# Kernel tuning notes

Measured on AMD Instinct MI355X. Metric: run time of the kernel, lower is better.

The kernel has to match this reference:

```python
import jax, jax.numpy as jnp
import numpy as np
from jax import lax

B, N, S, D1, D2 = 16, 4096, 1024, 128, 256
C_IN, C_MID, C_OUT = D1 + D2, 256, 128
BN_EPS = 1e-5


def setup_inputs() -> dict:
    key = jax.random.key(0)
    ks = jax.random.split(key, 12)
    return {
        "xyz1": jax.random.normal(ks[0], (B, N, 3), jnp.float32),
        "xyz2": jax.random.normal(ks[1], (B, S, 3), jnp.float32),
        "points1": jax.random.normal(ks[2], (B, N, D1), jnp.float32),
        "points2": jax.random.normal(ks[3], (B, S, D2), jnp.float32),
        # 1x1 Conv1d weights (kernel size 1 -> plain channel matmul)
        "W1": jax.random.normal(ks[4], (C_MID, C_IN), jnp.float32) * (1.0 / np.sqrt(C_IN)),
        "b1": jax.random.normal(ks[5], (C_MID,), jnp.float32) * 0.01,
        "g1": jnp.ones((C_MID,), jnp.float32),
        "be1": jnp.zeros((C_MID,), jnp.float32),
        "W2": jax.random.normal(ks[6], (C_OUT, C_MID), jnp.float32) * (1.0 / np.sqrt(C_MID)),
        "b2": jax.random.normal(ks[7], (C_OUT,), jnp.float32) * 0.01,
        "g2": jnp.ones((C_OUT,), jnp.float32),
        "be2": jnp.zeros((C_OUT,), jnp.float32),
    }


def _bn_relu(x, g, be):
    # BatchNorm1d in training mode: batch stats over (B, L) per channel, biased var
    mean = jnp.mean(x, axis=(0, 2), keepdims=True)
    var = jnp.var(x, axis=(0, 2), keepdims=True)
    y = (x - mean) * lax.rsqrt(var + BN_EPS)
    return jax.nn.relu(y * g[None, :, None] + be[None, :, None])


def reference(xyz1, xyz2, points1, points2, W1, b1, g1, be1, W2, b2, g2, be2):
    # squared pairwise distances [B,N,S] via ||a||^2 - 2ab + ||b||^2
    dist = (
        jnp.sum(xyz1 * xyz1, -1)[:, :, None]
        - 2.0 * jnp.einsum("bnd,bsd->bns", xyz1, xyz2)
        + jnp.sum(xyz2 * xyz2, -1)[:, None, :]
    )
    neg_d3, idx = lax.top_k(-dist, 3)            # 3 nearest neighbors
    d3 = -neg_d3                                  # [B,N,3]
    w = 1.0 / (d3 + 1e-8)
    w = w / jnp.sum(w, -1, keepdims=True)
    gathered = jax.vmap(lambda p, i: p[i])(points2, idx)   # [B,N,3,D2]
    interp = jnp.sum(gathered * w[..., None], axis=2)      # [B,N,D2]
    new_points = jnp.concatenate([points1, interp], axis=-1)  # [B,N,D1+D2]
    x = jnp.transpose(new_points, (0, 2, 1))                   # [B,C,N]
    x = _bn_relu(jnp.einsum("oc,bcn->bon", W1, x) + b1[None, :, None], g1, be1)
    x = _bn_relu(jnp.einsum("oc,bcn->bon", W2, x) + b2[None, :, None], g2, be2)
    return jnp.transpose(x, (0, 2, 1))                         # [B,N,C_OUT]
```

## Files before the change

### kernel.cpp

```cpp
#include <hip/hip_runtime.h>
#include <hip/hip_bf16.h>

#define NB    16
#define NPT   4096
#define NSRC  1024
#define ND1   128
#define ND2   256
#define NCIN  384
#define NCMID 256
#define NCOUT 128
#define BNTOT (NB * NPT)
#define BN_EPS 1e-5f

typedef float f32x4 __attribute__((ext_vector_type(4)));
typedef short bf16x8 __attribute__((ext_vector_type(8)));
typedef unsigned int uint;

union PK8 { unsigned short u[8]; uint4 q; };
union PK4 { unsigned short u[4]; uint2 q; };

static __device__ __forceinline__ unsigned short f2bf(float f) {
  __hip_bfloat16 h = __float2bfloat16(f);
  return __builtin_bit_cast(unsigned short, h);
}
static __device__ __forceinline__ float bf2f(unsigned short u) {
  return __builtin_bit_cast(float, (uint)u << 16);
}
static __device__ __forceinline__ void gl_lds16(const unsigned short* g, unsigned short* l) {
  __builtin_amdgcn_global_load_lds(
      (const __attribute__((address_space(1))) uint*)(const void*)g,
      (__attribute__((address_space(3))) uint*)(void*)l,
      16, 0, 0);
}

#if __has_builtin(__builtin_amdgcn_fmed3f)
#define MED3F(a, b, c) __builtin_amdgcn_fmed3f((a), (b), (c))
#else
#define MED3F(a, b, c) fmaxf((a), fminf((b), (c)))
#endif

static __device__ __forceinline__ bool prec(float da, int ia, float db, int ib) {
  return (da < db) || (da == db && ia < ib);
}

#define INSV(t0, t1, t2, j0, j1, j2, d, idx)                                   \
  {                                                                            \
    const bool c0 = (d) < t0;                                                  \
    const bool c1 = (d) < t1;                                                  \
    const bool c2 = (d) < t2;                                                  \
    const float m1 = MED3F(t0, t1, (d));                                       \
    const float m2 = fminf(t2, fmaxf(t1, (d)));                                \
    t0 = fminf(t0, (d));                                                       \
    j2 = c2 ? (c1 ? j1 : (idx)) : j2;                                          \
    j1 = c1 ? (c0 ? j0 : (idx)) : j1;                                          \
    j0 = c0 ? (idx) : j0;                                                      \
    t1 = m1; t2 = m2;                                                          \
  }

#define MERGE3(d0, j0, d1, j1, d2, j2, e0, i0, e1, i1, e2, i2)                 \
  {                                                                            \
    const bool p0 = prec(d0, j0, e0, i0);                                      \
    const float l0d = p0 ? e0 : d0; const int l0j = p0 ? i0 : j0;              \
    const float r0d = p0 ? d0 : e0; const int r0j = p0 ? j0 : i0;              \
    const bool p1 = prec(d1, j1, e1, i1);                                      \
    const float w1d = p1 ? d1 : e1; const int w1j = p1 ? j1 : i1;              \
    const bool pr1 = prec(l0d, l0j, w1d, w1j);                                 \
    const float r1d = pr1 ? l0d : w1d; const int r1j = pr1 ? l0j : w1j;        \
    const float q1d = pr1 ? w1d : l0d; const int q1j = pr1 ? w1j : l0j;        \
    const bool p2 = prec(d2, j2, e2, i2);                                      \
    const float w2d = p2 ? d2 : e2; const int w2j = p2 ? j2 : i2;              \
    const bool pr2 = prec(q1d, q1j, w2d, w2j);                                 \
    const float r2d = pr2 ? q1d : w2d; const int r2j = pr2 ? q1j : w2j;        \
    d0 = r0d; j0 = r0j; d1 = r1d; j1 = r1j; d2 = r2d; j2 = r2j;                \
  }

#define KNN_PAIR(i)                                                            \
  {                                                                            \
    const float4 va = n_slab[(i)];                                             \
    float da = va.w + n_a2;                                                    \
    da = fmaf(va.x, n_ax, da); da = fmaf(va.y, n_ay, da); da = fmaf(va.z, n_az, da); \
    INSV(n_ta0, n_ta1, n_ta2, n_ja0, n_ja1, n_ja2, da, n_qbase + (i));         \
    const float4 vb = n_slab[(i) + 1];                                         \
    float db = vb.w + n_a2;                                                    \
    db = fmaf(vb.x, n_ax, db); db = fmaf(vb.y, n_ay, db); db = fmaf(vb.z, n_az, db); \
    INSV(n_tb0, n_tb1, n_tb2, n_jb0, n_jb1, n_jb2, db, n_qbase + (i) + 1);     \
  }

__global__ __launch_bounds__(256) void prep_w_kernel(
    const float* __restrict__ w1, const float* __restrict__ w2,
    unsigned short* __restrict__ w1b, unsigned short* __restrict__ w2b)
{
  const int i = blockIdx.x * 256 + threadIdx.x;
  const bool isW1 = i < 24576;
  const float4 v = isW1 ? ((const float4*)w1)[i] : ((const float4*)w2)[i - 24576];
  PK4 pk;
  pk.u[0] = f2bf(v.x); pk.u[1] = f2bf(v.y); pk.u[2] = f2bf(v.z); pk.u[3] = f2bf(v.w);
  if (isW1) ((uint2*)w1b)[i] = pk.q;
  else      ((uint2*)w2b)[i - 24576] = pk.q;
}

__global__ __launch_bounds__(512, 4) void fg1_kernel(
    const float* __restrict__ xyz1, const float* __restrict__ xyz2,
    const float* __restrict__ points1, const float* __restrict__ points2,
    const unsigned short* __restrict__ W1bf, const float* __restrict__ bias1,
    unsigned short* __restrict__ h1bf, float* __restrict__ sum1, float* __restrict__ sq1)
{
  __shared__ unsigned short sA[2][128][32];
  __shared__ unsigned short sB[2][256][32];
  __shared__ float4 s2t[4 * 257];

  const int tid = threadIdx.x;
  const int lane = tid & 63;
  const int wave = tid >> 6;

  const int bid = (int)(blockIdx.x & 7) * 64 + (int)(blockIdx.x >> 3);
  const int ptBase = bid * 128;
  const int b = ptBase >> 12;

  const int fr = lane & 15;
  const int cs = lane >> 4;
  const int rdsh = ((cs ^ ((fr >> 1) & 3)) << 3);

  auto stageB = [&](int buf, int kt) {
    const int k0 = kt * 32;
#pragma unroll
    for (int c = 0; c < 2; ++c) {
      const int base = c * 512 + wave * 64;
      const int s = base + lane;
      const int row = s >> 2, c16 = s & 3;
      const int ks = c16 ^ ((row >> 1) & 3);
      gl_lds16(W1bf + (size_t)row * NCIN + k0 + ks * 8,
               &sB[buf][0][0] + base * 8);
    }
  };

  const float* g0p = points2;
  const float* g1p = points2;
  const float* g2p = points2;
  float gw0 = 0.f, gw1 = 0.f, gw2 = 0.f;

  auto stageA = [&](int buf, int kt) {
    const int row = tid >> 2, c16 = tid & 3;
    const int ks = c16 ^ ((row >> 1) & 3);
    const int k = kt * 32 + ks * 8;
    PK8 pk;
    if (k < ND1) {
      const float* src = points1 + (size_t)(ptBase + row) * ND1 + k;
      const float4 va = ((const float4*)src)[0];
      const float4 vb = ((const float4*)src)[1];
      pk.u[0] = f2bf(va.x); pk.u[1] = f2bf(va.y); pk.u[2] = f2bf(va.z); pk.u[3] = f2bf(va.w);
      pk.u[4] = f2bf(vb.x); pk.u[5] = f2bf(vb.y); pk.u[6] = f2bf(vb.z); pk.u[7] = f2bf(vb.w);
    } else {
      const int ko = k - ND1;
      const float4* r0 = (const float4*)(g0p + ko);
      const float4* r1 = (const float4*)(g1p + ko);
      const float4* r2 = (const float4*)(g2p + ko);
#pragma unroll
      for (int h = 0; h < 2; ++h) {
        const float4 va = r0[h], vb = r1[h], vc = r2[h];
        pk.u[h * 4 + 0] = f2bf(gw0 * va.x + gw1 * vb.x + gw2 * vc.x);
        pk.u[h * 4 + 1] = f2bf(gw0 * va.y + gw1 * vb.y + gw2 * vc.y);
        pk.u[h * 4 + 2] = f2bf(gw0 * va.z + gw1 * vb.z + gw2 * vc.z);
        pk.u[h * 4 + 3] = f2bf(gw0 * va.w + gw1 * vb.w + gw2 * vc.w);
      }
    }
    *(uint4*)(&sA[buf][0][0] + tid * 8) = pk.q;
  };

  const int ptl = tid >> 2;
  const float n_ax = xyz1[(size_t)(ptBase + ptl) * 3 + 0];
  const float n_ay = xyz1[(size_t)(ptBase + ptl) * 3 + 1];
  const float n_az = xyz1[(size_t)(ptBase + ptl) * 3 + 2];
  const float n_a2 = n_ax * n_ax + n_ay * n_ay + n_az * n_az;
  const float4* n_slab = &s2t[(tid & 3) * 257];
  const int n_qbase = (tid & 3) * 256;
  const float INF = 3.4e38f;
  float n_ta0 = INF, n_ta1 = INF, n_ta2 = INF;
  float n_tb0 = INF, n_tb1 = INF, n_tb2 = INF;
  int n_ja0 = 0, n_ja1 = 0, n_ja2 = 0, n_jb0 = 0, n_jb1 = 0, n_jb2 = 0;

  stageB(0, 0);
  if (tid < 256) {
    const float* src = xyz2 + (size_t)b * NSRC * 3 + tid * 12;
    const float4 l0 = ((const float4*)src)[0];
    const float4 l1 = ((const float4*)src)[1];
    const float4 l2 = ((const float4*)src)[2];
    const float xs[4] = {l0.x, l0.w, l1.z, l2.y};
    const float ys[4] = {l0.y, l1.x, l1.w, l2.z};
    const float zs[4] = {l0.z, l1.y, l2.x, l2.w};
    const int qq = tid >> 6;
    const int ibase = (tid & 63) * 4;
#pragma unroll
    for (int u = 0; u < 4; ++u) {
      const float c = xs[u] * xs[u] + ys[u] * ys[u] + zs[u] * zs[u];
      float4 v;
      v.x = -2.0f * xs[u]; v.y = -2.0f * ys[u]; v.z = -2.0f * zs[u]; v.w = c;
      s2t[qq * 257 + ibase + u] = v;
    }
  }
  stageA(0, 0);
  __syncthreads();

  f32x4 acc[16];
#pragma unroll
  for (int j = 0; j < 16; ++j)
#pragma unroll
    for (int q = 0; q < 4; ++q) acc[j][q] = 0.0f;

  int ki = 0;
  int buf = 0;
  for (int kt = 0; kt < 12; ++kt) {
    if (kt < 11) stageB(buf ^ 1, kt + 1);
    if (kt < 3) {
      const int take = (kt < 2) ? 43 : 42;
      for (int u = 0; u < take; ++u, ++ki) KNN_PAIR(2 * ki);
    } else if (kt == 3) {
      MERGE3(n_ta0, n_ja0, n_ta1, n_ja1, n_ta2, n_ja2,
             n_tb0, n_jb0, n_tb1, n_jb1, n_tb2, n_jb2);
#pragma unroll
      for (int m = 1; m <= 2; m <<= 1) {
        float e0 = __shfl_xor(n_ta0, m), e1 = __shfl_xor(n_ta1, m), e2 = __shfl_xor(n_ta2, m);
        int i0 = __shfl_xor(n_ja0, m), i1 = __shfl_xor(n_ja1, m), i2 = __shfl_xor(n_ja2, m);
        MERGE3(n_ta0, n_ja0, n_ta1, n_ja1, n_ta2, n_ja2, e0, i0, e1, i1, e2, i2);
      }
      float w0 = 1.f / (n_ta0 + 1e-8f), w1 = 1.f / (n_ta1 + 1e-8f), w2 = 1.f / (n_ta2 + 1e-8f);
      const float inv = 1.f / (w0 + w1 + w2);
      gw0 = w0 * inv; gw1 = w1 * inv; gw2 = w2 * inv;
      const float* p2base = points2 + (size_t)b * NSRC * ND2;
      g0p = p2base + (size_t)n_ja0 * ND2;
      g1p = p2base + (size_t)n_ja1 * ND2;
      g2p = p2base + (size_t)n_ja2 * ND2;
    }
    if (kt < 11) stageA(buf ^ 1, kt + 1);
    const bf16x8 a = *(const bf16x8*)&sA[buf][wave * 16 + fr][rdsh];
#pragma unroll
    for (int j = 0; j < 16; ++j) {
      const bf16x8 bv = *(const bf16x8*)&sB[buf][j * 16 + fr][rdsh];
      acc[j] = __builtin_amdgcn_mfma_f32_16x16x32_bf16(a, bv, acc[j], 0, 0, 0);
    }
    __syncthreads();
    buf ^= 1;
  }

  float* redS = (float*)&sA[0][0][0];
  float* redQ = redS + 2048;
  const int r0 = cs * 4;
#pragma unroll
  for (int j = 0; j < 16; ++j) {
    const int ch = j * 16 + fr;
    const float bb = bias1[ch];
    float s = 0.f, s2 = 0.f;
#pragma unroll
    for (int q = 0; q < 4; ++q) {
      const int pt = ptBase + wave * 16 + r0 + q;
      const float v = acc[j][q] + bb;
      h1bf[(size_t)pt * NCMID + ch] = f2bf(v);
      s += v; s2 += v * v;
    }
    s += __shfl_xor(s, 16);  s2 += __shfl_xor(s2, 16);
    s += __shfl_xor(s, 32);  s2 += __shfl_xor(s2, 32);
    if (cs == 0) { redS[wave * 256 + ch] = s; redQ[wave * 256 + ch] = s2; }
  }
  __syncthreads();
  if (tid < NCMID) {
    float s = 0.f, s2 = 0.f;
#pragma unroll
    for (int w = 0; w < 8; ++w) {
      s  += redS[w * 256 + tid];
      s2 += redQ[w * 256 + tid];
    }
    atomicAdd(&sum1[tid], s);
    atomicAdd(&sq1[tid], s2);
  }
}

template <int C>
__global__ void stats_kernel(const float* __restrict__ sum, const float* __restrict__ sumsq,
                             const float* __restrict__ g, const float* __restrict__ be,
                             float* __restrict__ a, float* __restrict__ d)
{
  const int c = threadIdx.x;
  const float mean = sum[c] * (1.0f / BNTOT);
  const float var = sumsq[c] * (1.0f / BNTOT) - mean * mean;
  const float inv = rsqrtf(var + BN_EPS);
  const float ac = g[c] * inv;
  a[c] = ac;
  d[c] = be[c] - mean * ac;
}

__global__ __launch_bounds__(256, 2) void gemm2_kernel(
    const unsigned short* __restrict__ h1bf, const unsigned short* __restrict__ W2bf,
    const float* __restrict__ bias2, const float* __restrict__ aff_a,
    const float* __restrict__ aff_d, unsigned short* __restrict__ h2bf,
    float* __restrict__ sum2, float* __restrict__ sq2)
{
  __shared__ unsigned short sA[2][128][32];
  __shared__ unsigned short sB[2][128][32];
  __shared__ float sa[NCMID], sd[NCMID];
  const int tid = threadIdx.x;
  const int lane = tid & 63;
  const int wave = tid >> 6;
  const int ptBase = blockIdx.x * 128;
  sa[tid] = aff_a[tid];
  sd[tid] = aff_d[tid];

  f32x4 acc[2][8];
#pragma unroll
  for (int m = 0; m < 2; ++m)
#pragma unroll
    for (int j = 0; j < 8; ++j)
#pragma unroll
      for (int q = 0; q < 4; ++q) acc[m][j][q] = 0.0f;

  const int fr = lane & 15;
  const int cs = lane >> 4;
  const int rdsh = ((cs ^ ((fr >> 1) & 3)) << 3);

  auto stageB = [&](int buf, int kt) {
    const int k0 = kt * 32;
#pragma unroll
    for (int c = 0; c < 2; ++c) {
      const int s = c * 256 + wave * 64 + lane;
      const int row = s >> 2, c16 = s & 3;
      const int ks = c16 ^ ((row >> 1) & 3);
      gl_lds16(W2bf + (size_t)row * NCMID + k0 + ks * 8,
               &sB[buf][0][0] + (c * 256 + wave * 64) * 8);
    }
  };
  auto stageA = [&](int buf, int kt) {
    const int k0 = kt * 32;
#pragma unroll
    for (int c = 0; c < 2; ++c) {
      const int s = c * 256 + tid;
      const int row = s >> 2, c16 = s & 3;
      const int ks = c16 ^ ((row >> 1) & 3);
      const int k = k0 + ks * 8;
      PK8 v;
      v.q = *(const uint4*)(h1bf + (size_t)(ptBase + row) * NCMID + k);
      PK8 pk;
#pragma unroll
      for (int j = 0; j < 8; ++j)
        pk.u[j] = f2bf(fmaxf(0.f, sa[k + j] * bf2f(v.u[j]) + sd[k + j]));
      *(uint4*)(&sA[buf][0][0] + s * 8) = pk.q;
    }
  };

  stageB(0, 0);
  __syncthreads();
  stageA(0, 0);
  __syncthreads();
  int cur = 0;
  for (int kt = 0; kt < 8; ++kt) {
    if (kt < 7) { stageB(cur ^ 1, kt + 1); stageA(cur ^ 1, kt + 1); }
    const bf16x8 a0 = *(const bf16x8*)&sA[cur][wave * 32 + fr][rdsh];
    const bf16x8 a1 = *(const bf16x8*)&sA[cur][wave * 32 + 16 + fr][rdsh];
#pragma unroll
    for (int j = 0; j < 8; ++j) {
      const bf16x8 b = *(const bf16x8*)&sB[cur][j * 16 + fr][rdsh];
      acc[0][j] = __builtin_amdgcn_mfma_f32_16x16x32_bf16(a0, b, acc[0][j], 0, 0, 0);
      acc[1][j] = __builtin_amdgcn_mfma_f32_16x16x32_bf16(a1, b, acc[1][j], 0, 0, 0);
    }
    __syncthreads();
    cur ^= 1;
  }

  float* redS = (float*)&sA[0][0][0];
  float* redQ = redS + 512;
  const int col = fr;
  const int r0 = cs * 4;
#pragma unroll
  for (int j = 0; j < 8; ++j) {
    const int ch = j * 16 + col;
    const float bb = bias2[ch];
    float s = 0.f, s2 = 0.f;
#pragma unroll
    for (int m = 0; m < 2; ++m)
#pragma unroll
      for (int q = 0; q < 4; ++q) {
        const int pt = ptBase + wave * 32 + m * 16 + r0 + q;
        const float v = acc[m][j][q] + bb;
        h2bf[(size_t)pt * NCOUT + ch] = f2bf(v);
        s += v; s2 += v * v;
      }
    s += __shfl_xor(s, 16);  s2 += __shfl_xor(s2, 16);
    s += __shfl_xor(s, 32);  s2 += __shfl_xor(s2, 32);
    if (cs == 0) { redS[wave * 128 + fr * 8 + j] = s; redQ[wave * 128 + fr * 8 + j] = s2; }
  }
  __syncthreads();
  if (tid < NCOUT) {
    const int ch = tid;
    const int f = ch & 15, j = ch >> 4;
    float s = 0.f, s2 = 0.f;
#pragma unroll
    for (int w = 0; w < 4; ++w) {
      s  += redS[w * 128 + f * 8 + j];
      s2 += redQ[w * 128 + f * 8 + j];
    }
    atomicAdd(&sum2[ch], s);
    atomicAdd(&sq2[ch], s2);
  }
}

__global__ __launch_bounds__(256) void final_kernel(
    const unsigned short* __restrict__ h2bf, float* __restrict__ out,
    const float* __restrict__ a2, const float* __restrict__ d2)
{
  __shared__ float sa[NCOUT], sd[NCOUT];
  if (threadIdx.x < NCOUT) { sa[threadIdx.x] = a2[threadIdx.x]; sd[threadIdx.x] = d2[threadIdx.x]; }
  __syncthreads();
  const int total8 = BNTOT * NCOUT / 8;
  for (int i = blockIdx.x * blockDim.x + threadIdx.x; i < total8;
       i += gridDim.x * blockDim.x) {
    PK8 v; v.q = ((const uint4*)h2bf)[i];
    const int c = (i & 15) * 8;
    float4 o0, o1;
    o0.x = fmaxf(0.f, sa[c + 0] * bf2f(v.u[0]) + sd[c + 0]);
    o0.y = fmaxf(0.f, sa[c + 1] * bf2f(v.u[1]) + sd[c + 1]);
    o0.z = fmaxf(0.f, sa[c + 2] * bf2f(v.u[2]) + sd[c + 2]);
    o0.w = fmaxf(0.f, sa[c + 3] * bf2f(v.u[3]) + sd[c + 3]);
    o1.x = fmaxf(0.f, sa[c + 4] * bf2f(v.u[4]) + sd[c + 4]);
    o1.y = fmaxf(0.f, sa[c + 5] * bf2f(v.u[5]) + sd[c + 5]);
    o1.z = fmaxf(0.f, sa[c + 6] * bf2f(v.u[6]) + sd[c + 6]);
    o1.w = fmaxf(0.f, sa[c + 7] * bf2f(v.u[7]) + sd[c + 7]);
    ((float4*)out)[i * 2]     = o0;
    ((float4*)out)[i * 2 + 1] = o1;
  }
}

extern "C" void kernel_launch(void* const* d_in, const int* in_sizes, int n_in,
                              void* d_out, int out_size, void* d_ws, size_t ws_size,
                              hipStream_t stream) {
  const float* xyz1    = (const float*)d_in[0];
  const float* xyz2    = (const float*)d_in[1];
  const float* points1 = (const float*)d_in[2];
  const float* points2 = (const float*)d_in[3];
  const float* W1      = (const float*)d_in[4];
  const float* b1      = (const float*)d_in[5];
  const float* g1      = (const float*)d_in[6];
  const float* be1     = (const float*)d_in[7];
  const float* W2      = (const float*)d_in[8];
  const float* b2      = (const float*)d_in[9];
  const float* g2      = (const float*)d_in[10];
  const float* be2     = (const float*)d_in[11];
  float* out = (float*)d_out;

  char* ws = (char*)d_ws;
  const size_t h1_bytes  = (size_t)BNTOT * NCMID * 2;
  const size_t h2_bytes  = (size_t)BNTOT * NCOUT * 2;
  const size_t w1b_bytes = (size_t)NCMID * NCIN * 2;
  const size_t w2b_bytes = (size_t)NCOUT * NCMID * 2;
  unsigned short* h1bf = (unsigned short*)ws;
  unsigned short* h2bf = (unsigned short*)(ws + h1_bytes);
  unsigned short* W1bf = (unsigned short*)(ws + h1_bytes + h2_bytes);
  unsigned short* W2bf = (unsigned short*)(ws + h1_bytes + h2_bytes + w1b_bytes);
  float* stats = (float*)(ws + h1_bytes + h2_bytes + w1b_bytes + w2b_bytes);
  float* sum1 = stats;
  float* sq1  = stats + 256;
  float* sum2 = stats + 512;
  float* sq2  = stats + 640;
  float* a1   = stats + 768;
  float* dd1  = stats + 1024;
  float* a2v  = stats + 1280;
  float* dd2v = stats + 1408;

  hipMemsetAsync(stats, 0, 768 * sizeof(float), stream);

  prep_w_kernel<<<128, 256, 0, stream>>>(W1, W2, W1bf, W2bf);
  fg1_kernel<<<BNTOT / 128, 512, 0, stream>>>(xyz1, xyz2, points1, points2,
                                              W1bf, b1, h1bf, sum1, sq1);
  stats_kernel<NCMID><<<1, NCMID, 0, stream>>>(sum1, sq1, g1, be1, a1, dd1);
  gemm2_kernel<<<BNTOT / 128, 256, 0, stream>>>(h1bf, W2bf, b2, a1, dd1, h2bf, sum2, sq2);
  stats_kernel<NCOUT><<<1, NCOUT, 0, stream>>>(sum2, sq2, g2, be2, a2v, dd2v);
  final_kernel<<<2048, 256, 0, stream>>>(h2bf, out, a2v, dd2v);
}
```

Baseline: 130.6 us.

## Restructure fused KNN+GEMM1 into smaller blocks with register A-fragments and partial-stat buffers

```diff
diff --git a/kernel.cpp b/kernel.cpp
--- a/kernel.cpp
+++ b/kernel.cpp
@@ -74,18 +74,6 @@
     d0 = r0d; j0 = r0j; d1 = r1d; j1 = r1j; d2 = r2d; j2 = r2j;                \
   }
 
-#define KNN_PAIR(i)                                                            \
-  {                                                                            \
-    const float4 va = n_slab[(i)];                                             \
-    float da = va.w + n_a2;                                                    \
-    da = fmaf(va.x, n_ax, da); da = fmaf(va.y, n_ay, da); da = fmaf(va.z, n_az, da); \
-    INSV(n_ta0, n_ta1, n_ta2, n_ja0, n_ja1, n_ja2, da, n_qbase + (i));         \
-    const float4 vb = n_slab[(i) + 1];                                         \
-    float db = vb.w + n_a2;                                                    \
-    db = fmaf(vb.x, n_ax, db); db = fmaf(vb.y, n_ay, db); db = fmaf(vb.z, n_az, db); \
-    INSV(n_tb0, n_tb1, n_tb2, n_jb0, n_jb1, n_jb2, db, n_qbase + (i) + 1);     \
-  }
-
 __global__ __launch_bounds__(256) void prep_w_kernel(
     const float* __restrict__ w1, const float* __restrict__ w2,
     unsigned short* __restrict__ w1b, unsigned short* __restrict__ w2b)
@@ -99,22 +87,21 @@
   else      ((uint2*)w2b)[i - 24576] = pk.q;
 }
 
-__global__ __launch_bounds__(512, 4) void fg1_kernel(
+__global__ __launch_bounds__(256, 4) void fg1_kernel(
     const float* __restrict__ xyz1, const float* __restrict__ xyz2,
     const float* __restrict__ points1, const float* __restrict__ points2,
     const unsigned short* __restrict__ W1bf, const float* __restrict__ bias1,
-    unsigned short* __restrict__ h1bf, float* __restrict__ sum1, float* __restrict__ sq1)
-{
-  __shared__ unsigned short sA[2][128][32];
+    unsigned short* __restrict__ h1bf, float* __restrict__ pS, float* __restrict__ pQ)
+{
   __shared__ unsigned short sB[2][256][32];
-  __shared__ float4 s2t[4 * 257];
+  float4* s2t = (float4*)&sB[1][0][0];
 
   const int tid = threadIdx.x;
   const int lane = tid & 63;
   const int wave = tid >> 6;
 
-  const int bid = (int)(blockIdx.x & 7) * 64 + (int)(blockIdx.x >> 3);
-  const int ptBase = bid * 128;
+  const int bid = (int)(blockIdx.x & 7) * 128 + (int)(blockIdx.x >> 3);
+  const int ptBase = bid * 64;
   const int b = ptBase >> 12;
 
   const int fr = lane & 15;
@@ -124,63 +111,17 @@
   auto stageB = [&](int buf, int kt) {
     const int k0 = kt * 32;
 #pragma unroll
-    for (int c = 0; c < 2; ++c) {
-      const int base = c * 512 + wave * 64;
+    for (int c = 0; c < 4; ++c) {
+      const int base = c * 256 + wave * 64;
       const int s = base + lane;
       const int row = s >> 2, c16 = s & 3;
       const int ks = c16 ^ ((row >> 1) & 3);
-      gl_lds16(W1bf + (size_t)row * NCIN + k0 + ks * 8,
-               &sB[buf][0][0] + base * 8);
+      gl_lds16(W1bf + (size_t)row * NCIN + k0 + ks * 8, &sB[buf][0][0] + base * 8);
     }
   };
 
-  const float* g0p = points2;
-  const float* g1p = points2;
-  const float* g2p = points2;
-  float gw0 = 0.f, gw1 = 0.f, gw2 = 0.f;
-
-  auto stageA = [&](int buf, int kt) {
-    const int row = tid >> 2, c16 = tid & 3;
-    const int ks = c16 ^ ((row >> 1) & 3);
-    const int k = kt * 32 + ks * 8;
-    PK8 pk;
-    if (k < ND1) {
-      const float* src = points1 + (size_t)(ptBase + row) * ND1 + k;
-      const float4 va = ((const float4*)src)[0];
-      const float4 vb = ((const float4*)src)[1];
-      pk.u[0] = f2bf(va.x); pk.u[1] = f2bf(va.y); pk.u[2] = f2bf(va.z); pk.u[3] = f2bf(va.w);
-      pk.u[4] = f2bf(vb.x); pk.u[5] = f2bf(vb.y); pk.u[6] = f2bf(vb.z); pk.u[7] = f2bf(vb.w);
-    } else {
-      const int ko = k - ND1;
-      const float4* r0 = (const float4*)(g0p + ko);
-      const float4* r1 = (const float4*)(g1p + ko);
-      const float4* r2 = (const float4*)(g2p + ko);
-#pragma unroll
-      for (int h = 0; h < 2; ++h) {
-        const float4 va = r0[h], vb = r1[h], vc = r2[h];
-        pk.u[h * 4 + 0] = f2bf(gw0 * va.x + gw1 * vb.x + gw2 * vc.x);
-        pk.u[h * 4 + 1] = f2bf(gw0 * va.y + gw1 * vb.y + gw2 * vc.y);
-        pk.u[h * 4 + 2] = f2bf(gw0 * va.z + gw1 * vb.z + gw2 * vc.z);
-        pk.u[h * 4 + 3] = f2bf(gw0 * va.w + gw1 * vb.w + gw2 * vc.w);
-      }
-    }
-    *(uint4*)(&sA[buf][0][0] + tid * 8) = pk.q;
-  };
-
-  const int ptl = tid >> 2;
-  const float n_ax = xyz1[(size_t)(ptBase + ptl) * 3 + 0];
-  const float n_ay = xyz1[(size_t)(ptBase + ptl) * 3 + 1];
-  const float n_az = xyz1[(size_t)(ptBase + ptl) * 3 + 2];
-  const float n_a2 = n_ax * n_ax + n_ay * n_ay + n_az * n_az;
-  const float4* n_slab = &s2t[(tid & 3) * 257];
-  const int n_qbase = (tid & 3) * 256;
-  const float INF = 3.4e38f;
-  float n_ta0 = INF, n_ta1 = INF, n_ta2 = INF;
-  float n_tb0 = INF, n_tb1 = INF, n_tb2 = INF;
-  int n_ja0 = 0, n_ja1 = 0, n_ja2 = 0, n_jb0 = 0, n_jb1 = 0, n_jb2 = 0;
-
   stageB(0, 0);
-  if (tid < 256) {
+  {
     const float* src = xyz2 + (size_t)b * NSRC * 3 + tid * 12;
     const float4 l0 = ((const float4*)src)[0];
     const float4 l1 = ((const float4*)src)[1];
@@ -188,51 +129,100 @@
     const float xs[4] = {l0.x, l0.w, l1.z, l2.y};
     const float ys[4] = {l0.y, l1.x, l1.w, l2.z};
     const float zs[4] = {l0.z, l1.y, l2.x, l2.w};
-    const int qq = tid >> 6;
-    const int ibase = (tid & 63) * 4;
 #pragma unroll
     for (int u = 0; u < 4; ++u) {
+      const int s = tid * 4 + u;
+      const int qq = s >> 8, ii = s & 255;
       const float c = xs[u] * xs[u] + ys[u] * ys[u] + zs[u] * zs[u];
       float4 v;
       v.x = -2.0f * xs[u]; v.y = -2.0f * ys[u]; v.z = -2.0f * zs[u]; v.w = c;
-      s2t[qq * 257 + ibase + u] = v;
-    }
-  }
-  stageA(0, 0);
+      s2t[qq * 256 + (ii ^ qq)] = v;
+    }
+  }
+  __syncthreads();
+
+  const int ptl = tid >> 2;
+  const int q = tid & 3;
+  const float n_ax = xyz1[(size_t)(ptBase + ptl) * 3 + 0];
+  const float n_ay = xyz1[(size_t)(ptBase + ptl) * 3 + 1];
+  const float n_az = xyz1[(size_t)(ptBase + ptl) * 3 + 2];
+  const float n_a2 = n_ax * n_ax + n_ay * n_ay + n_az * n_az;
+  const float4* n_slab = &s2t[q * 256];
+  const int n_qbase = q * 256;
+  const float INF = 3.4e38f;
+  float n_ta0 = INF, n_ta1 = INF, n_ta2 = INF;
+  float n_tb0 = INF, n_tb1 = INF, n_tb2 = INF;
+  int n_ja0 = 0, n_ja1 = 0, n_ja2 = 0, n_jb0 = 0, n_jb1 = 0, n_jb2 = 0;
+
+  for (int i = 0; i < 256; i += 2) {
+    const float4 va = n_slab[i ^ q];
+    float da = va.w + n_a2;
+    da = fmaf(va.x, n_ax, da); da = fmaf(va.y, n_ay, da); da = fmaf(va.z, n_az, da);
+    INSV(n_ta0, n_ta1, n_ta2, n_ja0, n_ja1, n_ja2, da, n_qbase + i);
+    const float4 vb = n_slab[(i + 1) ^ q];
+    float db = vb.w + n_a2;
+    db = fmaf(vb.x, n_ax, db); db = fmaf(vb.y, n_ay, db); db = fmaf(vb.z, n_az, db);
+    INSV(n_tb0, n_tb1, n_tb2, n_jb0, n_jb1, n_jb2, db, n_qbase + i + 1);
+  }
+  MERGE3(n_ta0, n_ja0, n_ta1, n_ja1, n_ta2, n_ja2,
+         n_tb0, n_jb0, n_tb1, n_jb1, n_tb2, n_jb2);
+#pragma unroll
+  for (int m = 1; m <= 2; m <<= 1) {
+    float e0 = __shfl_xor(n_ta0, m), e1 = __shfl_xor(n_ta1, m), e2 = __shfl_xor(n_ta2, m);
+    int i0 = __shfl_xor(n_ja0, m), i1 = __shfl_xor(n_ja1, m), i2 = __shfl_xor(n_ja2, m);
+    MERGE3(n_ta0, n_ja0, n_ta1, n_ja1, n_ta2, n_ja2, e0, i0, e1, i1, e2, i2);
+  }
+  float wq0 = 1.f / (n_ta0 + 1e-8f), wq1 = 1.f / (n_ta1 + 1e-8f), wq2 = 1.f / (n_ta2 + 1e-8f);
+  const float winv = 1.f / (wq0 + wq1 + wq2);
+  wq0 *= winv; wq1 *= winv; wq2 *= winv;
+
+  const int srcl = 4 * fr;
+  const int j0r = __shfl(n_ja0, srcl);
+  const int j1r = __shfl(n_ja1, srcl);
+  const int j2r = __shfl(n_ja2, srcl);
+  const float gw0 = __shfl(wq0, srcl);
+  const float gw1 = __shfl(wq1, srcl);
+  const float gw2 = __shfl(wq2, srcl);
+  const float* p2base = points2 + (size_t)b * NSRC * ND2;
+  const float* g0p = p2base + (size_t)j0r * ND2;
+  const float* g1p = p2base + (size_t)j1r * ND2;
+  const float* g2p = p2base + (size_t)j2r * ND2;
+
   __syncthreads();
 
   f32x4 acc[16];
 #pragma unroll
   for (int j = 0; j < 16; ++j)
 #pragma unroll
-    for (int q = 0; q < 4; ++q) acc[j][q] = 0.0f;
-
-  int ki = 0;
+    for (int p = 0; p < 4; ++p) acc[j][p] = 0.0f;
+
+  const int arow = ptBase + wave * 16 + fr;
   int buf = 0;
   for (int kt = 0; kt < 12; ++kt) {
     if (kt < 11) stageB(buf ^ 1, kt + 1);
-    if (kt < 3) {
-      const int take = (kt < 2) ? 43 : 42;
-      for (int u = 0; u < take; ++u, ++ki) KNN_PAIR(2 * ki);
-    } else if (kt == 3) {
-      MERGE3(n_ta0, n_ja0, n_ta1, n_ja1, n_ta2, n_ja2,
-             n_tb0, n_jb0, n_tb1, n_jb1, n_tb2, n_jb2);
-#pragma unroll
-      for (int m = 1; m <= 2; m <<= 1) {
-        float e0 = __shfl_xor(n_ta0, m), e1 = __shfl_xor(n_ta1, m), e2 = __shfl_xor(n_ta2, m);
-        int i0 = __shfl_xor(n_ja0, m), i1 = __shfl_xor(n_ja1, m), i2 = __shfl_xor(n_ja2, m);
-        MERGE3(n_ta0, n_ja0, n_ta1, n_ja1, n_ta2, n_ja2, e0, i0, e1, i1, e2, i2);
+    const int k = kt * 32 + cs * 8;
+    PK8 af;
+    if (kt < 4) {
+      const float* src = points1 + (size_t)arow * ND1 + k;
+      const float4 va = ((const float4*)src)[0];
+      const float4 vb = ((const float4*)src)[1];
+      af.u[0] = f2bf(va.x); af.u[1] = f2bf(va.y); af.u[2] = f2bf(va.z); af.u[3] = f2bf(va.w);
+      af.u[4] = f2bf(vb.x); af.u[5] = f2bf(vb.y); af.u[6] = f2bf(vb.z); af.u[7] = f2bf(vb.w);
+    } else {
+      const int ko = k - ND1;
+      const float4* r0 = (const float4*)(g0p + ko);
+      const float4* r1 = (const float4*)(g1p + ko);
+      const float4* r2 = (const float4*)(g2p + ko);
+#pragma unroll
+      for (int h = 0; h < 2; ++h) {
+        const float4 va = r0[h], vb = r1[h], vc = r2[h];
+        af.u[h * 4 + 0] = f2bf(gw0 * va.x + gw1 * vb.x + gw2 * vc.x);
+        af.u[h * 4 + 1] = f2bf(gw0 * va.y + gw1 * vb.y + gw2 * vc.y);
+        af.u[h * 4 + 2] = f2bf(gw0 * va.z + gw1 * vb.z + gw2 * vc.z);
+        af.u[h * 4 + 3] = f2bf(gw0 * va.w + gw1 * vb.w + gw2 * vc.w);
       }
-      float w0 = 1.f / (n_ta0 + 1e-8f), w1 = 1.f / (n_ta1 + 1e-8f), w2 = 1.f / (n_ta2 + 1e-8f);
-      const float inv = 1.f / (w0 + w1 + w2);
-      gw0 = w0 * inv; gw1 = w1 * inv; gw2 = w2 * inv;
-      const float* p2base = points2 + (size_t)b * NSRC * ND2;
-      g0p = p2base + (size_t)n_ja0 * ND2;
-      g1p = p2base + (size_t)n_ja1 * ND2;
-      g2p = p2base + (size_t)n_ja2 * ND2;
-    }
-    if (kt < 11) stageA(buf ^ 1, kt + 1);
-    const bf16x8 a = *(const bf16x8*)&sA[buf][wave * 16 + fr][rdsh];
+    }
+    const bf16x8 a = __builtin_bit_cast(bf16x8, af.q);
 #pragma unroll
     for (int j = 0; j < 16; ++j) {
       const bf16x8 bv = *(const bf16x8*)&sB[buf][j * 16 + fr][rdsh];
@@ -242,8 +232,8 @@
     buf ^= 1;
   }
 
-  float* redS = (float*)&sA[0][0][0];
-  float* redQ = redS + 2048;
+  float* redS = (float*)&sB[0][0][0];
+  float* redQ = redS + 1024;
   const int r0 = cs * 4;
 #pragma unroll
   for (int j = 0; j < 16; ++j) {
@@ -251,9 +241,9 @@
     const float bb = bias1[ch];
     float s = 0.f, s2 = 0.f;
 #pragma unroll
-    for (int q = 0; q < 4; ++q) {
-      const int pt = ptBase + wave * 16 + r0 + q;
-      const float v = acc[j][q] + bb;
+    for (int p = 0; p < 4; ++p) {
+      const int pt = ptBase + wave * 16 + r0 + p;
+      const float v = acc[j][p] + bb;
       h1bf[(size_t)pt * NCMID + ch] = f2bf(v);
       s += v; s2 += v * v;
     }
@@ -262,16 +252,28 @@
     if (cs == 0) { redS[wave * 256 + ch] = s; redQ[wave * 256 + ch] = s2; }
   }
   __syncthreads();
-  if (tid < NCMID) {
-    float s = 0.f, s2 = 0.f;
-#pragma unroll
-    for (int w = 0; w < 8; ++w) {
-      s  += redS[w * 256 + tid];
-      s2 += redQ[w * 256 + tid];
-    }
-    atomicAdd(&sum1[tid], s);
-    atomicAdd(&sq1[tid], s2);
-  }
+  {
+    const int ch = tid;
+    const float s  = redS[ch] + redS[256 + ch] + redS[512 + ch] + redS[768 + ch];
+    const float s2 = redQ[ch] + redQ[256 + ch] + redQ[512 + ch] + redQ[768 + ch];
+    pS[(size_t)bid * NCMID + ch] = s;
+    pQ[(size_t)bid * NCMID + ch] = s2;
+  }
+}
+
+__global__ __launch_bounds__(256) void colred_kernel(
+    const float* __restrict__ pS, const float* __restrict__ pQ,
+    float* __restrict__ sum1, float* __restrict__ sq1)
+{
+  const int ch = threadIdx.x;
+  const int r0 = blockIdx.x * 32;
+  float s = 0.f, s2 = 0.f;
+  for (int i = 0; i < 32; ++i) {
+    s  += pS[(size_t)(r0 + i) * NCMID + ch];
+    s2 += pQ[(size_t)(r0 + i) * NCMID + ch];
+  }
+  atomicAdd(&sum1[ch], s);
+  atomicAdd(&sq1[ch], s2);
 }
 
 template <int C>
@@ -449,11 +451,14 @@
   const size_t h2_bytes  = (size_t)BNTOT * NCOUT * 2;
   const size_t w1b_bytes = (size_t)NCMID * NCIN * 2;
   const size_t w2b_bytes = (size_t)NCOUT * NCMID * 2;
+  const size_t ps_bytes  = (size_t)1024 * NCMID * 4;
   unsigned short* h1bf = (unsigned short*)ws;
   unsigned short* h2bf = (unsigned short*)(ws + h1_bytes);
   unsigned short* W1bf = (unsigned short*)(ws + h1_bytes + h2_bytes);
   unsigned short* W2bf = (unsigned short*)(ws + h1_bytes + h2_bytes + w1b_bytes);
-  float* stats = (float*)(ws + h1_bytes + h2_bytes + w1b_bytes + w2b_bytes);
+  float* pS = (float*)(ws + h1_bytes + h2_bytes + w1b_bytes + w2b_bytes);
+  float* pQ = (float*)(ws + h1_bytes + h2_bytes + w1b_bytes + w2b_bytes + ps_bytes);
+  float* stats = (float*)(ws + h1_bytes + h2_bytes + w1b_bytes + w2b_bytes + 2 * ps_bytes);
   float* sum1 = stats;
   float* sq1  = stats + 256;
   float* sum2 = stats + 512;
@@ -466,8 +471,9 @@
   hipMemsetAsync(stats, 0, 768 * sizeof(float), stream);
 
   prep_w_kernel<<<128, 256, 0, stream>>>(W1, W2, W1bf, W2bf);
-  fg1_kernel<<<BNTOT / 128, 512, 0, stream>>>(xyz1, xyz2, points1, points2,
-                                              W1bf, b1, h1bf, sum1, sq1);
+  fg1_kernel<<<1024, 256, 0, stream>>>(xyz1, xyz2, points1, points2,
+                                       W1bf, b1, h1bf, pS, pQ);
+  colred_kernel<<<32, 256, 0, stream>>>(pS, pQ, sum1, sq1);
   stats_kernel<NCMID><<<1, NCMID, 0, stream>>>(sum1, sq1, g1, be1, a1, dd1);
   gemm2_kernel<<<BNTOT / 128, 256, 0, stream>>>(h1bf, W2bf, b2, a1, dd1, h2bf, sum2, sq2);
   stats_kernel<NCOUT><<<1, NCOUT, 0, stream>>>(sum2, sq2, g2, be2, a2v, dd2v);
```

New measurement: 133.9 us. +2.5%, slower.

## Split fused KNN+GEMM1 kernel into separate KNN and GEMM1 kernels

Applied to the files above, without the earlier changes.

```diff
diff --git a/kernel.cpp b/kernel.cpp
--- a/kernel.cpp
+++ b/kernel.cpp
@@ -74,18 +74,6 @@
     d0 = r0d; j0 = r0j; d1 = r1d; j1 = r1j; d2 = r2d; j2 = r2j;                \
   }
 
-#define KNN_PAIR(i)                                                            \
-  {                                                                            \
-    const float4 va = n_slab[(i)];                                             \
-    float da = va.w + n_a2;                                                    \
-    da = fmaf(va.x, n_ax, da); da = fmaf(va.y, n_ay, da); da = fmaf(va.z, n_az, da); \
-    INSV(n_ta0, n_ta1, n_ta2, n_ja0, n_ja1, n_ja2, da, n_qbase + (i));         \
-    const float4 vb = n_slab[(i) + 1];                                         \
-    float db = vb.w + n_a2;                                                    \
-    db = fmaf(vb.x, n_ax, db); db = fmaf(vb.y, n_ay, db); db = fmaf(vb.z, n_az, db); \
-    INSV(n_tb0, n_tb1, n_tb2, n_jb0, n_jb1, n_jb2, db, n_qbase + (i) + 1);     \
-  }
-
 __global__ __launch_bounds__(256) void prep_w_kernel(
     const float* __restrict__ w1, const float* __restrict__ w2,
     unsigned short* __restrict__ w1b, unsigned short* __restrict__ w2b)
@@ -99,22 +87,97 @@
   else      ((uint2*)w2b)[i - 24576] = pk.q;
 }
 
-__global__ __launch_bounds__(512, 4) void fg1_kernel(
+__global__ __launch_bounds__(256) void knn_kernel(
     const float* __restrict__ xyz1, const float* __restrict__ xyz2,
+    int* __restrict__ nidx, float* __restrict__ nwgt)
+{
+  __shared__ float4 s2t[NSRC];
+  __shared__ float md[64][4][3];
+  __shared__ int   mj[64][4][3];
+  const int tid = threadIdx.x;
+  const int lane = tid & 63;
+  const int wave = tid >> 6;
+  const int ptBase = blockIdx.x * 64;
+  const int b = ptBase >> 12;
+
+  {
+    const float* src = xyz2 + (size_t)b * NSRC * 3 + tid * 12;
+    const float4 l0 = ((const float4*)src)[0];
+    const float4 l1 = ((const float4*)src)[1];
+    const float4 l2 = ((const float4*)src)[2];
+    const float xs[4] = {l0.x, l0.w, l1.z, l2.y};
+    const float ys[4] = {l0.y, l1.x, l1.w, l2.z};
+    const float zs[4] = {l0.z, l1.y, l2.x, l2.w};
+#pragma unroll
+    for (int u = 0; u < 4; ++u) {
+      const float c = xs[u] * xs[u] + ys[u] * ys[u] + zs[u] * zs[u];
+      float4 v;
+      v.x = -2.0f * xs[u]; v.y = -2.0f * ys[u]; v.z = -2.0f * zs[u]; v.w = c;
+      s2t[tid * 4 + u] = v;
+    }
+  }
+  __syncthreads();
+
+  const int p = ptBase + lane;
+  const float ax = xyz1[(size_t)p * 3 + 0];
+  const float ay = xyz1[(size_t)p * 3 + 1];
+  const float az = xyz1[(size_t)p * 3 + 2];
+  const float a2 = ax * ax + ay * ay + az * az;
+  const float4* slab = &s2t[wave * 256];
+  const int qbase = wave * 256;
+
+  const float INF = 3.4e38f;
+  float t0 = INF, t1 = INF, t2 = INF;
+  int j0 = 0, j1 = 0, j2 = 0;
+#pragma unroll 4
+  for (int i = 0; i < 256; ++i) {
+    const float4 v = slab[i];
+    float d = v.w + a2;
+    d = fmaf(v.x, ax, d); d = fmaf(v.y, ay, d); d = fmaf(v.z, az, d);
+    INSV(t0, t1, t2, j0, j1, j2, d, qbase + i);
+  }
+  md[lane][wave][0] = t0; md[lane][wave][1] = t1; md[lane][wave][2] = t2;
+  mj[lane][wave][0] = j0; mj[lane][wave][1] = j1; mj[lane][wave][2] = j2;
+  __syncthreads();
+
+  if (tid < 64) {
+    float d0 = md[tid][0][0], d1 = md[tid][0][1], d2 = md[tid][0][2];
+    int   i0 = mj[tid][0][0], i1 = mj[tid][0][1], i2 = mj[tid][0][2];
+#pragma unroll
+    for (int w = 1; w < 4; ++w) {
+      const float e0 = md[tid][w][0], e1 = md[tid][w][1], e2 = md[tid][w][2];
+      const int   k0 = mj[tid][w][0], k1 = mj[tid][w][1], k2 = mj[tid][w][2];
+      MERGE3(d0, i0, d1, i1, d2, i2, e0, k0, e1, k1, e2, k2);
+    }
+    const int pp = ptBase + tid;
+    float w0 = 1.f / (d0 + 1e-8f), w1 = 1.f / (d1 + 1e-8f), w2 = 1.f / (d2 + 1e-8f);
+    const float inv = 1.f / (w0 + w1 + w2);
+    nidx[(size_t)pp * 3 + 0] = i0;
+    nidx[(size_t)pp * 3 + 1] = i1;
+    nidx[(size_t)pp * 3 + 2] = i2;
+    nwgt[(size_t)pp * 3 + 0] = w0 * inv;
+    nwgt[(size_t)pp * 3 + 1] = w1 * inv;
+    nwgt[(size_t)pp * 3 + 2] = w2 * inv;
+  }
+}
+
+__global__ __launch_bounds__(256, 3) void gemm1_kernel(
     const float* __restrict__ points1, const float* __restrict__ points2,
+    const int* __restrict__ nidx, const float* __restrict__ nwgt,
     const unsigned short* __restrict__ W1bf, const float* __restrict__ bias1,
     unsigned short* __restrict__ h1bf, float* __restrict__ sum1, float* __restrict__ sq1)
 {
-  __shared__ unsigned short sA[2][128][32];
+  __shared__ unsigned short sA[2][64][32];
   __shared__ unsigned short sB[2][256][32];
-  __shared__ float4 s2t[4 * 257];
+  __shared__ int   sj[64][3];
+  __shared__ float sw[64][3];
 
   const int tid = threadIdx.x;
   const int lane = tid & 63;
   const int wave = tid >> 6;
 
-  const int bid = (int)(blockIdx.x & 7) * 64 + (int)(blockIdx.x >> 3);
-  const int ptBase = bid * 128;
+  const int bid = (int)(blockIdx.x & 7) * 128 + (int)(blockIdx.x >> 3);
+  const int ptBase = bid * 64;
   const int b = ptBase >> 12;
 
   const int fr = lane & 15;
@@ -124,13 +187,12 @@
   auto stageB = [&](int buf, int kt) {
     const int k0 = kt * 32;
 #pragma unroll
-    for (int c = 0; c < 2; ++c) {
-      const int base = c * 512 + wave * 64;
+    for (int c = 0; c < 4; ++c) {
+      const int base = c * 256 + wave * 64;
       const int s = base + lane;
       const int row = s >> 2, c16 = s & 3;
       const int ks = c16 ^ ((row >> 1) & 3);
-      gl_lds16(W1bf + (size_t)row * NCIN + k0 + ks * 8,
-               &sB[buf][0][0] + base * 8);
+      gl_lds16(W1bf + (size_t)row * NCIN + k0 + ks * 8, &sB[buf][0][0] + base * 8);
     }
   };
 
@@ -167,71 +229,36 @@
     *(uint4*)(&sA[buf][0][0] + tid * 8) = pk.q;
   };
 
-  const int ptl = tid >> 2;
-  const float n_ax = xyz1[(size_t)(ptBase + ptl) * 3 + 0];
-  const float n_ay = xyz1[(size_t)(ptBase + ptl) * 3 + 1];
-  const float n_az = xyz1[(size_t)(ptBase + ptl) * 3 + 2];
-  const float n_a2 = n_ax * n_ax + n_ay * n_ay + n_az * n_az;
-  const float4* n_slab = &s2t[(tid & 3) * 257];
-  const int n_qbase = (tid & 3) * 256;
-  const float INF = 3.4e38f;
-  float n_ta0 = INF, n_ta1 = INF, n_ta2 = INF;
-  float n_tb0 = INF, n_tb1 = INF, n_tb2 = INF;
-  int n_ja0 = 0, n_ja1 = 0, n_ja2 = 0, n_jb0 = 0, n_jb1 = 0, n_jb2 = 0;
-
   stageB(0, 0);
-  if (tid < 256) {
-    const float* src = xyz2 + (size_t)b * NSRC * 3 + tid * 12;
-    const float4 l0 = ((const float4*)src)[0];
-    const float4 l1 = ((const float4*)src)[1];
-    const float4 l2 = ((const float4*)src)[2];
-    const float xs[4] = {l0.x, l0.w, l1.z, l2.y};
-    const float ys[4] = {l0.y, l1.x, l1.w, l2.z};
-    const float zs[4] = {l0.z, l1.y, l2.x, l2.w};
-    const int qq = tid >> 6;
-    const int ibase = (tid & 63) * 4;
-#pragma unroll
-    for (int u = 0; u < 4; ++u) {
-      const float c = xs[u] * xs[u] + ys[u] * ys[u] + zs[u] * zs[u];
-      float4 v;
-      v.x = -2.0f * xs[u]; v.y = -2.0f * ys[u]; v.z = -2.0f * zs[u]; v.w = c;
-      s2t[qq * 257 + ibase + u] = v;
-    }
+  if (tid < 64) {
+    const int pp = ptBase + tid;
+    sj[tid][0] = nidx[(size_t)pp * 3 + 0];
+    sj[tid][1] = nidx[(size_t)pp * 3 + 1];
+    sj[tid][2] = nidx[(size_t)pp * 3 + 2];
+    sw[tid][0] = nwgt[(size_t)pp * 3 + 0];
+    sw[tid][1] = nwgt[(size_t)pp * 3 + 1];
+    sw[tid][2] = nwgt[(size_t)pp * 3 + 2];
   }
   stageA(0, 0);
   __syncthreads();
+  {
+    const int row = tid >> 2;
+    const float* p2base = points2 + (size_t)b * NSRC * ND2;
+    g0p = p2base + (size_t)sj[row][0] * ND2;
+    g1p = p2base + (size_t)sj[row][1] * ND2;
+    g2p = p2base + (size_t)sj[row][2] * ND2;
+    gw0 = sw[row][0]; gw1 = sw[row][1]; gw2 = sw[row][2];
+  }
 
   f32x4 acc[16];
 #pragma unroll
   for (int j = 0; j < 16; ++j)
 #pragma unroll
-    for (int q = 0; q < 4; ++q) acc[j][q] = 0.0f;
-
-  int ki = 0;
+    for (int p = 0; p < 4; ++p) acc[j][p] = 0.0f;
+
   int buf = 0;
   for (int kt = 0; kt < 12; ++kt) {
-    if (kt < 11) stageB(buf ^ 1, kt + 1);
-    if (kt < 3) {
-      const int take = (kt < 2) ? 43 : 42;
-      for (int u = 0; u < take; ++u, ++ki) KNN_PAIR(2 * ki);
-    } else if (kt == 3) {
-      MERGE3(n_ta0, n_ja0, n_ta1, n_ja1, n_ta2, n_ja2,
-             n_tb0, n_jb0, n_tb1, n_jb1, n_tb2, n_jb2);
-#pragma unroll
-      for (int m = 1; m <= 2; m <<= 1) {
-        float e0 = __shfl_xor(n_ta0, m), e1 = __shfl_xor(n_ta1, m), e2 = __shfl_xor(n_ta2, m);
-        int i0 = __shfl_xor(n_ja0, m), i1 = __shfl_xor(n_ja1, m), i2 = __shfl_xor(n_ja2, m);
-        MERGE3(n_ta0, n_ja0, n_ta1, n_ja1, n_ta2, n_ja2, e0, i0, e1, i1, e2, i2);
-      }
-      float w0 = 1.f / (n_ta0 + 1e-8f), w1 = 1.f / (n_ta1 + 1e-8f), w2 = 1.f / (n_ta2 + 1e-8f);
-      const float inv = 1.f / (w0 + w1 + w2);
-      gw0 = w0 * inv; gw1 = w1 * inv; gw2 = w2 * inv;
-      const float* p2base = points2 + (size_t)b * NSRC * ND2;
-      g0p = p2base + (size_t)n_ja0 * ND2;
-      g1p = p2base + (size_t)n_ja1 * ND2;
-      g2p = p2base + (size_t)n_ja2 * ND2;
-    }
-    if (kt < 11) stageA(buf ^ 1, kt + 1);
+    if (kt < 11) { stageB(buf ^ 1, kt + 1); stageA(buf ^ 1, kt + 1); }
     const bf16x8 a = *(const bf16x8*)&sA[buf][wave * 16 + fr][rdsh];
 #pragma unroll
     for (int j = 0; j < 16; ++j) {
@@ -243,7 +270,7 @@
   }
 
   float* redS = (float*)&sA[0][0][0];
-  float* redQ = redS + 2048;
+  float* redQ = redS + 1024;
   const int r0 = cs * 4;
 #pragma unroll
   for (int j = 0; j < 16; ++j) {
@@ -251,9 +278,9 @@
     const float bb = bias1[ch];
     float s = 0.f, s2 = 0.f;
 #pragma unroll
-    for (int q = 0; q < 4; ++q) {
-      const int pt = ptBase + wave * 16 + r0 + q;
-      const float v = acc[j][q] + bb;
+    for (int p = 0; p < 4; ++p) {
+      const int pt = ptBase + wave * 16 + r0 + p;
+      const float v = acc[j][p] + bb;
       h1bf[(size_t)pt * NCMID + ch] = f2bf(v);
       s += v; s2 += v * v;
     }
@@ -262,15 +289,12 @@
     if (cs == 0) { redS[wave * 256 + ch] = s; redQ[wave * 256 + ch] = s2; }
   }
   __syncthreads();
-  if (tid < NCMID) {
-    float s = 0.f, s2 = 0.f;
-#pragma unroll
-    for (int w = 0; w < 8; ++w) {
-      s  += redS[w * 256 + tid];
-      s2 += redQ[w * 256 + tid];
-    }
-    atomicAdd(&sum1[tid], s);
-    atomicAdd(&sq1[tid], s2);
+  {
+    const int ch = tid;
+    const float s  = redS[ch] + redS[256 + ch] + redS[512 + ch] + redS[768 + ch];
+    const float s2 = redQ[ch] + redQ[256 + ch] + redQ[512 + ch] + redQ[768 + ch];
+    atomicAdd(&sum1[ch], s);
+    atomicAdd(&sq1[ch], s2);
   }
 }
 
@@ -449,11 +473,14 @@
   const size_t h2_bytes  = (size_t)BNTOT * NCOUT * 2;
   const size_t w1b_bytes = (size_t)NCMID * NCIN * 2;
   const size_t w2b_bytes = (size_t)NCOUT * NCMID * 2;
+  const size_t idx_bytes = (size_t)BNTOT * 3 * 4;
   unsigned short* h1bf = (unsigned short*)ws;
   unsigned short* h2bf = (unsigned short*)(ws + h1_bytes);
   unsigned short* W1bf = (unsigned short*)(ws + h1_bytes + h2_bytes);
   unsigned short* W2bf = (unsigned short*)(ws + h1_bytes + h2_bytes + w1b_bytes);
-  float* stats = (float*)(ws + h1_bytes + h2_bytes + w1b_bytes + w2b_bytes);
+  int*   nidx = (int*)(ws + h1_bytes + h2_bytes + w1b_bytes + w2b_bytes);
+  float* nwgt = (float*)(ws + h1_bytes + h2_bytes + w1b_bytes + w2b_bytes + idx_bytes);
+  float* stats = (float*)(ws + h1_bytes + h2_bytes + w1b_bytes + w2b_bytes + 2 * idx_bytes);
   float* sum1 = stats;
   float* sq1  = stats + 256;
   float* sum2 = stats + 512;
@@ -466,8 +493,9 @@
   hipMemsetAsync(stats, 0, 768 * sizeof(float), stream);
 
   prep_w_kernel<<<128, 256, 0, stream>>>(W1, W2, W1bf, W2bf);
-  fg1_kernel<<<BNTOT / 128, 512, 0, stream>>>(xyz1, xyz2, points1, points2,
-                                              W1bf, b1, h1bf, sum1, sq1);
+  knn_kernel<<<BNTOT / 64, 256, 0, stream>>>(xyz1, xyz2, nidx, nwgt);
+  gemm1_kernel<<<BNTOT / 64, 256, 0, stream>>>(points1, points2, nidx, nwgt,
+                                               W1bf, b1, h1bf, sum1, sq1);
   stats_kernel<NCMID><<<1, NCMID, 0, stream>>>(sum1, sq1, g1, be1, a1, dd1);
   gemm2_kernel<<<BNTOT / 128, 256, 0, stream>>>(h1bf, W2bf, b2, a1, dd1, h2bf, sum2, sq2);
   stats_kernel<NCOUT><<<1, NCOUT, 0, stream>>>(sum2, sq2, g2, be2, a2v, dd2v);
```

New measurement: 141.6 us. 8.4% more time.
